# Kernel tuning notes

Measured on AMD Instinct MI355X. Metric: run time of the kernel, lower is better.

The kernel has to match this reference:

```python
import jax, jax.numpy as jnp
import numpy as np

N_NODES = 50000
N_EDGES = 800000
N_GRAPHS = 64
EPS = 1e-12


def setup_inputs() -> dict:
    key = jax.random.key(0)
    ks = jax.random.split(key, 8)
    x = jax.random.normal(ks[0], (N_NODES, 128), dtype=jnp.float32)
    edge_index = jax.random.randint(ks[1], (2, N_EDGES), 0, N_NODES, dtype=jnp.int64)
    batch = jnp.sort(jax.random.randint(ks[2], (N_NODES,), 0, N_GRAPHS, dtype=jnp.int64))
    W1 = jax.random.normal(ks[3], (128, 64), dtype=jnp.float32) * 0.1
    W2 = jax.random.normal(ks[4], (64, 64), dtype=jnp.float32) * 0.1
    W3 = jax.random.normal(ks[5], (64, 64), dtype=jnp.float32) * 0.1
    Wl = jax.random.normal(ks[6], (128, 32), dtype=jnp.float32) * 0.1
    return {
        'x': x, 'edge_index': edge_index, 'batch': batch,
        'W1': W1, 'b1': jnp.zeros((64,), jnp.float32),
        'W2': W2, 'b2': jnp.zeros((64,), jnp.float32),
        'W3': W3, 'b3': jnpp if False else jnp.zeros((64,), jnp.float32),
        'Wl': Wl, 'bl': jnp.zeros((32,), jnp.float32),
    }


def _gcn_conv(h, W, b, src, dst, dinv, enorm, n):
    # PyG GCNConv: D^-1/2 (A+I) D^-1/2 (h W) + b, self-loops included analytically
    hw = h @ W
    agg = jax.ops.segment_sum(hw[src] * enorm[:, None], dst, num_segments=n)
    agg = agg + (dinv * dinv)[:, None] * hw  # self-loop term
    return agg + b


def _norm_relu(h):
    # F.normalize(p=2, dim=1) then relu
    nrm = jnp.sqrt(jnp.sum(h * h, axis=1, keepdims=True))
    return jax.nn.relu(h / jnp.maximum(nrm, EPS))


def reference(x, edge_index, batch, W1, b1, W2, b2, W3, b3, Wl, bl):
    n = x.shape[0]
    src, dst = edge_index[0], edge_index[1]
    # degree with self-loops (counts incoming edges at target, +1 for self-loop)
    deg = jax.ops.segment_sum(jnp.ones((src.shape[0],), x.dtype), dst, num_segments=n) + 1.0
    dinv = 1.0 / jnp.sqrt(deg)
    enorm = dinv[src] * dinv[dst]

    h = _norm_relu(_gcn_conv(x, W1, b1, src, dst, dinv, enorm, n))
    h = _norm_relu(_gcn_conv(h, W2, b2, src, dst, dinv, enorm, n))
    h = _norm_relu(_gcn_conv(h, W3, b3, src, dst, dinv, enorm, n))

    counts = jax.ops.segment_sum(jnp.ones((n,), x.dtype), batch, num_segments=N_GRAPHS)
    x_mean = jax.ops.segment_sum(h, batch, num_segments=N_GRAPHS) / jnp.maximum(counts, 1.0)[:, None]
    x_max = jax.ops.segment_max(h, batch, num_segments=N_GRAPHS)
    x_max = jnp.where(counts[:, None] > 0, x_max, 0.0)  # guard empty graphs

    pooled = jnp.concatenate([x_mean, x_max], axis=-1)  # [B, 2*hidden]
    return pooled @ Wl + bl
```

## Files before the change

kernel.cpp:

```cpp
#include <hip/hip_runtime.h>
#include <hip/hip_bf16.h>

#define N_NODES 50000
#define N_EDGES 800000
#define N_GRAPHS 64
#define HID 64
#define SCAN_NB 196
#define FILL_RANGES 8
#define RANGE_SIZE ((N_NODES + FILL_RANGES - 1) / FILL_RANGES)
#define MM1_BLOCKS ((N_NODES + 63) / 64)
#define FILL_BLOCKS (FILL_RANGES * ((N_EDGES + 255) / 256))

static inline size_t align256(size_t x) { return (x + 255) & ~(size_t)255; }

typedef __attribute__((ext_vector_type(8))) short short8v;
typedef __attribute__((ext_vector_type(4))) float f32x4;

__device__ __forceinline__ unsigned short f2bf(float f) {
    unsigned int u = __float_as_uint(f);
    unsigned int r = (u + 0x7fffu + ((u >> 16) & 1u)) >> 16;
    return (unsigned short)r;
}
__device__ __forceinline__ float bf2f(unsigned short h) {
    return __uint_as_float(((unsigned int)h) << 16);
}

__global__ void zero2(int* __restrict__ a, int na, int* __restrict__ b, int nb) {
    int i = blockIdx.x * blockDim.x + threadIdx.x;
    if (i < na) a[i] = 0;
    else if (i < na + nb) b[i - na] = 0;
}

__global__ void deg_kernel(const int* __restrict__ ei, int* __restrict__ cnt) {
    int e = blockIdx.x * blockDim.x + threadIdx.x;
    if (e < N_EDGES) atomicAdd(&cnt[ei[N_EDGES + e]], 1);
}

__global__ __launch_bounds__(256) void scan_a(const int* __restrict__ cnt,
                                              int* __restrict__ incl,
                                              int* __restrict__ bsum) {
    __shared__ int sd[256];
    int t = threadIdx.x;
    int i = blockIdx.x * 256 + t;
    int v = (i < N_NODES) ? cnt[i] : 0;
    sd[t] = v;
    __syncthreads();
    for (int off = 1; off < 256; off <<= 1) {
        int u = (t >= off) ? sd[t - off] : 0;
        __syncthreads();
        sd[t] += u;
        __syncthreads();
    }
    if (i < N_NODES) incl[i] = sd[t];
    if (t == 255) bsum[blockIdx.x] = sd[255];
}

__global__ __launch_bounds__(384) void scan_b_gstart(const int* __restrict__ bsum,
                                                     int* __restrict__ boff,
                                                     const int* __restrict__ batch,
                                                     int* __restrict__ gstart) {
    __shared__ int sd[256];
    int t = threadIdx.x;
    int v = 0;
    if (t < 256) {
        v = (t < SCAN_NB) ? bsum[t] : 0;
        sd[t] = v;
    }
    __syncthreads();
    for (int off = 1; off < 256; off <<= 1) {
        int u = (t < 256 && t >= off) ? sd[t - off] : 0;
        __syncthreads();
        if (t < 256) sd[t] += u;
        __syncthreads();
    }
    if (t < SCAN_NB) boff[t] = sd[t] - v;
    if (t >= 256 && t - 256 <= N_GRAPHS) {
        int g = t - 256;
        int lo = 0, hi = N_NODES;
        while (lo < hi) {
            int mid = (lo + hi) >> 1;
            if (batch[mid] < g) lo = mid + 1; else hi = mid;
        }
        gstart[g] = lo;
    }
}

__global__ void scan_c(const int* __restrict__ cnt, const int* __restrict__ incl,
                       const int* __restrict__ boff, int* __restrict__ row_ptr,
                       int* __restrict__ fill_ptr, float* __restrict__ dinv) {
    int i = blockIdx.x * blockDim.x + threadIdx.x;
    if (i < N_NODES) {
        int c = cnt[i];
        int run = boff[i >> 8] + incl[i];
        row_ptr[i + 1] = run;
        fill_ptr[i] = run - c;
        dinv[i] = rsqrtf((float)c + 1.0f);
        if (i == 0) row_ptr[0] = 0;
    }
}

__global__ __launch_bounds__(256) void fill_mm1_kernel(const int* __restrict__ ei,
                                                       int* __restrict__ fill_ptr,
                                                       unsigned short* __restrict__ csr_src,
                                                       const float* __restrict__ h,
                                                       const float* __restrict__ W,
                                                       const float* __restrict__ dinv,
                                                       unsigned short* __restrict__ hw2) {
    constexpr int K = 128;
    constexpr int NSTEP = K / 32;
    __shared__ unsigned short sWH[NSTEP * 4 * 64 * 8];
    __shared__ unsigned short sWL[NSTEP * 4 * 64 * 8];
    int tid = threadIdx.x;

    if (blockIdx.x >= MM1_BLOCKS) {
        int fb = blockIdx.x - MM1_BLOCKS;
        int r = fb & (FILL_RANGES - 1);
        int e = (fb >> 3) * 256 + tid;
        if (e >= N_EDGES) return;
        int dst = ei[N_EDGES + e];
        int lo = r * RANGE_SIZE;
        if (dst >= lo && dst < lo + RANGE_SIZE) {
            int src = ei[e];
            int pos = atomicAdd(&fill_ptr[dst], 1);
            csr_src[pos] = (unsigned short)src;
        }
        return;
    }

    int r0 = blockIdx.x * 64;
#pragma unroll 1
    for (int ent = tid; ent < NSTEP * 4 * 64; ent += 256) {
        int lane_e = ent & 63;
        int c = (ent >> 6) & 3;
        int step = ent >> 8;
        int kb = step * 32 + (lane_e >> 4) * 8;
        int n = c * 16 + (lane_e & 15);
#pragma unroll
        for (int j = 0; j < 8; ++j) {
            float f = W[(kb + j) * 64 + n];
            unsigned short hi = f2bf(f);
            sWH[ent * 8 + j] = hi;
            sWL[ent * 8 + j] = f2bf(f - bf2f(hi));
        }
    }
    __syncthreads();

    int lane = tid & 63;
    int wid = tid >> 6;
    int arow = min(r0 + wid * 16 + (lane & 15), N_NODES - 1);
    const float* ap = h + (size_t)arow * K;
    int klane = (lane >> 4) * 8;

    f32x4 acc[4];
#pragma unroll
    for (int c = 0; c < 4; ++c) acc[c] = (f32x4){0.f, 0.f, 0.f, 0.f};

#pragma unroll 1
    for (int step = 0; step < NSTEP; ++step) {
        int kb = step * 32 + klane;
        float4 f0 = *(const float4*)&ap[kb];
        float4 f1 = *(const float4*)&ap[kb + 4];
        float fv[8] = {f0.x, f0.y, f0.z, f0.w, f1.x, f1.y, f1.z, f1.w};
        short8v ahi, alo;
#pragma unroll
        for (int j = 0; j < 8; ++j) {
            unsigned short hi = f2bf(fv[j]);
            ahi[j] = (short)hi;
            alo[j] = (short)f2bf(fv[j] - bf2f(hi));
        }
#pragma unroll
        for (int c = 0; c < 4; ++c) {
            short8v bh = *(const short8v*)&sWH[((step * 4 + c) * 64 + lane) * 8];
            short8v bl = *(const short8v*)&sWL[((step * 4 + c) * 64 + lane) * 8];
            acc[c] = __builtin_amdgcn_mfma_f32_16x16x32_bf16(ahi, bh, acc[c], 0, 0, 0);
            acc[c] = __builtin_amdgcn_mfma_f32_16x16x32_bf16(alo, bh, acc[c], 0, 0, 0);
            acc[c] = __builtin_amdgcn_mfma_f32_16x16x32_bf16(ahi, bl, acc[c], 0, 0, 0);
        }
    }

    int rb = r0 + wid * 16 + (lane >> 4) * 4;
#pragma unroll
    for (int j = 0; j < 4; ++j) {
        int row = rb + j;
        if (row < N_NODES) {
            float dv = dinv[row];
#pragma unroll
            for (int c = 0; c < 4; ++c) {
                hw2[(size_t)row * 64 + c * 16 + (lane & 15)] = f2bf(dv * acc[c][j]);
            }
        }
    }
}

template <int K>
__global__ __launch_bounds__(256) void mfma_matmul(const float* __restrict__ h,
                                                   const float* __restrict__ W,
                                                   const float* __restrict__ dinv,
                                                   unsigned short* __restrict__ hw2) {
    constexpr int NSTEP = K / 32;
    __shared__ unsigned short sWH[NSTEP * 4 * 64 * 8];
    __shared__ unsigned short sWL[NSTEP * 4 * 64 * 8];
    int tid = threadIdx.x;
    int r0 = blockIdx.x * 64;

#pragma unroll 1
    for (int ent = tid; ent < NSTEP * 4 * 64; ent += 256) {
        int lane_e = ent & 63;
        int c = (ent >> 6) & 3;
        int step = ent >> 8;
        int kb = step * 32 + (lane_e >> 4) * 8;
        int n = c * 16 + (lane_e & 15);
#pragma unroll
        for (int j = 0; j < 8; ++j) {
            float f = W[(kb + j) * 64 + n];
            unsigned short hi = f2bf(f);
            sWH[ent * 8 + j] = hi;
            sWL[ent * 8 + j] = f2bf(f - bf2f(hi));
        }
    }
    __syncthreads();

    int lane = tid & 63;
    int wid = tid >> 6;
    int arow = min(r0 + wid * 16 + (lane & 15), N_NODES - 1);
    const float* ap = h + (size_t)arow * K;
    int klane = (lane >> 4) * 8;

    f32x4 acc[4];
#pragma unroll
    for (int c = 0; c < 4; ++c) acc[c] = (f32x4){0.f, 0.f, 0.f, 0.f};

#pragma unroll 1
    for (int step = 0; step < NSTEP; ++step) {
        int kb = step * 32 + klane;
        float4 f0 = *(const float4*)&ap[kb];
        float4 f1 = *(const float4*)&ap[kb + 4];
        float fv[8] = {f0.x, f0.y, f0.z, f0.w, f1.x, f1.y, f1.z, f1.w};
        short8v ahi, alo;
#pragma unroll
        for (int j = 0; j < 8; ++j) {
            unsigned short hi = f2bf(fv[j]);
            ahi[j] = (short)hi;
            alo[j] = (short)f2bf(fv[j] - bf2f(hi));
        }
#pragma unroll
        for (int c = 0; c < 4; ++c) {
            short8v bh = *(const short8v*)&sWH[((step * 4 + c) * 64 + lane) * 8];
            short8v bl = *(const short8v*)&sWL[((step * 4 + c) * 64 + lane) * 8];
            acc[c] = __builtin_amdgcn_mfma_f32_16x16x32_bf16(ahi, bh, acc[c], 0, 0, 0);
            acc[c] = __builtin_amdgcn_mfma_f32_16x16x32_bf16(alo, bh, acc[c], 0, 0, 0);
            acc[c] = __builtin_amdgcn_mfma_f32_16x16x32_bf16(ahi, bl, acc[c], 0, 0, 0);
        }
    }

    int rb = r0 + wid * 16 + (lane >> 4) * 4;
#pragma unroll
    for (int j = 0; j < 4; ++j) {
        int row = rb + j;
        if (row < N_NODES) {
            float dv = dinv[row];
#pragma unroll
            for (int c = 0; c < 4; ++c) {
                hw2[(size_t)row * 64 + c * 16 + (lane & 15)] = f2bf(dv * acc[c][j]);
            }
        }
    }
}

template <bool POOL>
__global__ __launch_bounds__(256) void agg_kernel(const unsigned short* __restrict__ hw2,
                                                  const int* __restrict__ row_ptr,
                                                  const unsigned short* __restrict__ csr_src,
                                                  const float* __restrict__ dinv,
                                                  const float* __restrict__ b,
                                                  float* __restrict__ hout,
                                                  const int* __restrict__ batch,
                                                  float* __restrict__ gsum,
                                                  float* __restrict__ gmax) {
    __shared__ float sh[4][64];
    int tid = threadIdx.x;
    int node = blockIdx.x * 4 + (tid >> 6);
    int lane = tid & 63;
    int grp = lane >> 3;
    int gl  = lane & 7;
    int s = row_ptr[node], e = row_ptr[node + 1];

    float acc[8] = {0.f, 0.f, 0.f, 0.f, 0.f, 0.f, 0.f, 0.f};
    for (int base = s; base < e; base += 64) {
        int nE = min(64, e - base);
        int msrc = (lane < nE) ? (int)csr_src[base + lane] : 0;
#pragma unroll
        for (int rr = 0; rr < 8; ++rr) {
            int i = rr * 8;
            if (i >= nE) break;
            int myi = i + grp;
            int src = __shfl(msrc, myi, 64);
            bool ok = myi < nE;
            int srcx = ok ? src : node;
            short8v v = *(const short8v*)&hw2[(size_t)srcx * 64 + gl * 8];
            if (ok) {
#pragma unroll
                for (int j = 0; j < 8; ++j) acc[j] += bf2f((unsigned short)v[j]);
            }
        }
    }
#pragma unroll
    for (int off = 8; off <= 32; off <<= 1) {
#pragma unroll
        for (int j = 0; j < 8; ++j) acc[j] += __shfl_xor(acc[j], off, 64);
    }
    short8v sv = *(const short8v*)&hw2[(size_t)node * 64 + gl * 8];
#pragma unroll
    for (int j = 0; j < 8; ++j) acc[j] += bf2f((unsigned short)sv[j]);

    float di = dinv[node];
    float4 b0 = *(const float4*)&b[gl * 8];
    float4 b1 = *(const float4*)&b[gl * 8 + 4];
    float val[8];
    val[0] = di * acc[0] + b0.x;
    val[1] = di * acc[1] + b0.y;
    val[2] = di * acc[2] + b0.z;
    val[3] = di * acc[3] + b0.w;
    val[4] = di * acc[4] + b1.x;
    val[5] = di * acc[5] + b1.y;
    val[6] = di * acc[6] + b1.z;
    val[7] = di * acc[7] + b1.w;

    float sq = 0.f;
#pragma unroll
    for (int j = 0; j < 8; ++j) sq += val[j] * val[j];
#pragma unroll
    for (int off = 1; off <= 4; off <<= 1) sq += __shfl_xor(sq, off, 64);
    float inv = 1.0f / fmaxf(sqrtf(sq), 1e-12f);

    if (POOL) {
        if (grp == 0) {
            float4 r0, r1;
            r0.x = fmaxf(val[0] * inv, 0.f);
            r0.y = fmaxf(val[1] * inv, 0.f);
            r0.z = fmaxf(val[2] * inv, 0.f);
            r0.w = fmaxf(val[3] * inv, 0.f);
            r1.x = fmaxf(val[4] * inv, 0.f);
            r1.y = fmaxf(val[5] * inv, 0.f);
            r1.z = fmaxf(val[6] * inv, 0.f);
            r1.w = fmaxf(val[7] * inv, 0.f);
            *(float4*)&sh[tid >> 6][gl * 8] = r0;
            *(float4*)&sh[tid >> 6][gl * 8 + 4] = r1;
        }
        __syncthreads();
        if (tid < 64) {
            int nb = blockIdx.x * 4;
            int gcur = batch[nb];
            float runsum = 0.f, runmax = 0.f;
#pragma unroll
            for (int w = 0; w < 4; ++w) {
                int g = batch[nb + w];
                if (g != gcur) {
                    atomicAdd(&gsum[gcur * 64 + tid], runsum);
                    atomicMax((int*)&gmax[gcur * 64 + tid], __float_as_int(runmax));
                    runsum = 0.f; runmax = 0.f; gcur = g;
                }
                float v = sh[w][tid];
                runsum += v;
                runmax = fmaxf(runmax, v);
            }
            atomicAdd(&gsum[gcur * 64 + tid], runsum);
            atomicMax((int*)&gmax[gcur * 64 + tid], __float_as_int(runmax));
        }
    } else {
        if (grp == 0) {
            float4 r0, r1;
            r0.x = fmaxf(val[0] * inv, 0.f);
            r0.y = fmaxf(val[1] * inv, 0.f);
            r0.z = fmaxf(val[2] * inv, 0.f);
            r0.w = fmaxf(val[3] * inv, 0.f);
            r1.x = fmaxf(val[4] * inv, 0.f);
            r1.y = fmaxf(val[5] * inv, 0.f);
            r1.z = fmaxf(val[6] * inv, 0.f);
            r1.w = fmaxf(val[7] * inv, 0.f);
            *(float4*)&hout[(size_t)node * 64 + gl * 8] = r0;
            *(float4*)&hout[(size_t)node * 64 + gl * 8 + 4] = r1;
        }
    }
}

__global__ __launch_bounds__(128) void linear_kernel(const float* __restrict__ gsum,
                                                     const float* __restrict__ gmax,
                                                     const int* __restrict__ gstart,
                                                     const float* __restrict__ Wl,
                                                     const float* __restrict__ bl,
                                                     float* __restrict__ out) {
    int g = blockIdx.x;
    __shared__ float pooled[128];
    int t = threadIdx.x;
    if (t < 64) {
        int cnt = gstart[g + 1] - gstart[g];
        pooled[t] = gsum[g * 64 + t] / fmaxf((float)cnt, 1.0f);
    } else {
        pooled[t] = gmax[g * 64 + (t - 64)];
    }
    __syncthreads();
    if (t < 32) {
        float acc = bl[t];
#pragma unroll 8
        for (int k = 0; k < 128; ++k) acc += pooled[k] * Wl[k * 32 + t];
        out[g * 32 + t] = acc;
    }
}

extern "C" void kernel_launch(void* const* d_in, const int* in_sizes, int n_in,
                              void* d_out, int out_size, void* d_ws, size_t ws_size,
                              hipStream_t stream) {
    const float* x        = (const float*)d_in[0];
    const int*   ei       = (const int*)d_in[1];
    const int*   batch    = (const int*)d_in[2];
    const float* W1       = (const float*)d_in[3];
    const float* b1       = (const float*)d_in[4];
    const float* W2       = (const float*)d_in[5];
    const float* b2       = (const float*)d_in[6];
    const float* W3       = (const float*)d_in[7];
    const float* b3       = (const float*)d_in[8];
    const float* Wl       = (const float*)d_in[9];
    const float* bl       = (const float*)d_in[10];
    float* out = (float*)d_out;

    char* ws = (char*)d_ws;
    int*   cnt      = (int*)ws;                 ws += align256((size_t)N_NODES * 4);
    int*   incl     = (int*)ws;                 ws += align256((size_t)N_NODES * 4);
    int*   bsum     = (int*)ws;                 ws += align256((size_t)SCAN_NB * 4);
    int*   boff     = (int*)ws;                 ws += align256((size_t)SCAN_NB * 4);
    int*   row_ptr  = (int*)ws;                 ws += align256((size_t)(N_NODES + 1) * 4);
    int*   fill_ptr = (int*)ws;                 ws += align256((size_t)N_NODES * 4);
    float* dinv     = (float*)ws;               ws += align256((size_t)N_NODES * 4);
    int*   gstart   = (int*)ws;                 ws += align256((size_t)(N_GRAPHS + 1) * 4);
    float* gsum     = (float*)ws;               ws += (size_t)N_GRAPHS * 64 * 4;
    float* gmax     = (float*)ws;               ws += align256((size_t)N_GRAPHS * 64 * 4);
    unsigned short* csr_src = (unsigned short*)ws; ws += align256((size_t)N_EDGES * 2);
    unsigned short* hwb = (unsigned short*)ws;  ws += align256((size_t)N_NODES * 64 * 2);
    float* h1       = (float*)ws;               ws += align256((size_t)N_NODES * 64 * 4);
    float* h2       = (float*)ws;               ws += align256((size_t)N_NODES * 64 * 4);

    hipLaunchKernelGGL(zero2, dim3((N_NODES + 2 * N_GRAPHS * 64 + 255) / 256), dim3(256), 0,
                       stream, cnt, N_NODES, (int*)gsum, 2 * N_GRAPHS * 64);
    hipLaunchKernelGGL(deg_kernel, dim3((N_EDGES + 255) / 256), dim3(256), 0, stream, ei, cnt);
    hipLaunchKernelGGL(scan_a, dim3(SCAN_NB), dim3(256), 0, stream, cnt, incl, bsum);
    hipLaunchKernelGGL(scan_b_gstart, dim3(1), dim3(384), 0, stream, bsum, boff, batch, gstart);
    hipLaunchKernelGGL(scan_c, dim3(SCAN_NB), dim3(256), 0, stream,
                       cnt, incl, boff, row_ptr, fill_ptr, dinv);

    const int mm_grid = (N_NODES + 63) / 64;
    const int agg_grid = N_NODES / 4;

    hipLaunchKernelGGL(fill_mm1_kernel, dim3(MM1_BLOCKS + FILL_BLOCKS), dim3(256), 0, stream,
                       ei, fill_ptr, csr_src, x, W1, dinv, hwb);

    hipLaunchKernelGGL((agg_kernel<false>), dim3(agg_grid), dim3(256), 0, stream,
                       hwb, row_ptr, csr_src, dinv, b1, h1, batch, gsum, gmax);
    hipLaunchKernelGGL((mfma_matmul<64>), dim3(mm_grid), dim3(256), 0, stream, h1, W2, dinv, hwb);
    hipLaunchKernelGGL((agg_kernel<false>), dim3(agg_grid), dim3(256), 0, stream,
                       hwb, row_ptr, csr_src, dinv, b2, h2, batch, gsum, gmax);
    hipLaunchKernelGGL((mfma_matmul<64>), dim3(mm_grid), dim3(256), 0, stream, h2, W3, dinv, hwb);
    hipLaunchKernelGGL((agg_kernel<true>), dim3(agg_grid), dim3(256), 0, stream,
                       hwb, row_ptr, csr_src, dinv, b3, (float*)nullptr, batch, gsum, gmax);

    hipLaunchKernelGGL(linear_kernel, dim3(N_GRAPHS), dim3(128), 0, stream,
                       gsum, gmax, gstart, Wl, bl, out);
}
```

Measured before the change: 208.8 us.

## Fuse GCN aggregation with next-layer matmul in one kernel

Merges each layer's aggregation, normalize and ReLU with the following layer's MFMA matmul. Each 1024-thread block aggregates 16 nodes into shared memory, then 4 waves multiply that 16x64 tile by the next weight matrix. This removes the fp32 intermediate h1/h2 round trips through global memory and two kernel launches. In exchange every block re-converts W into shared memory, and the large blocks with a barrier may lower occupancy and make waves wait on the slowest node's neighbor loop.

```diff
diff --git a/kernel.cpp b/kernel.cpp
--- a/kernel.cpp
+++ b/kernel.cpp
@@ -192,19 +192,20 @@
     }
 }
 
-template <int K>
-__global__ __launch_bounds__(256) void mfma_matmul(const float* __restrict__ h,
-                                                   const float* __restrict__ W,
-                                                   const float* __restrict__ dinv,
-                                                   unsigned short* __restrict__ hw2) {
-    constexpr int NSTEP = K / 32;
-    __shared__ unsigned short sWH[NSTEP * 4 * 64 * 8];
-    __shared__ unsigned short sWL[NSTEP * 4 * 64 * 8];
+__global__ __launch_bounds__(1024) void aggmm_kernel(const unsigned short* __restrict__ hw_in,
+                                                     const int* __restrict__ row_ptr,
+                                                     const unsigned short* __restrict__ csr_src,
+                                                     const float* __restrict__ dinv,
+                                                     const float* __restrict__ b,
+                                                     const float* __restrict__ Wn,
+                                                     unsigned short* __restrict__ hw_out) {
+    __shared__ unsigned short sWH[2 * 4 * 64 * 8];
+    __shared__ unsigned short sWL[2 * 4 * 64 * 8];
+    __shared__ float hlds[16 * 68];
     int tid = threadIdx.x;
-    int r0 = blockIdx.x * 64;
-
-#pragma unroll 1
-    for (int ent = tid; ent < NSTEP * 4 * 64; ent += 256) {
+
+    if (tid < 512) {
+        int ent = tid;
         int lane_e = ent & 63;
         int c = (ent >> 6) & 3;
         int step = ent >> 8;
@@ -212,74 +213,15 @@
         int n = c * 16 + (lane_e & 15);
 #pragma unroll
         for (int j = 0; j < 8; ++j) {
-            float f = W[(kb + j) * 64 + n];
+            float f = Wn[(kb + j) * 64 + n];
             unsigned short hi = f2bf(f);
             sWH[ent * 8 + j] = hi;
             sWL[ent * 8 + j] = f2bf(f - bf2f(hi));
         }
     }
-    __syncthreads();
-
-    int lane = tid & 63;
+
     int wid = tid >> 6;
-    int arow = min(r0 + wid * 16 + (lane & 15), N_NODES - 1);
-    const float* ap = h + (size_t)arow * K;
-    int klane = (lane >> 4) * 8;
-
-    f32x4 acc[4];
-#pragma unroll
-    for (int c = 0; c < 4; ++c) acc[c] = (f32x4){0.f, 0.f, 0.f, 0.f};
-
-#pragma unroll 1
-    for (int step = 0; step < NSTEP; ++step) {
-        int kb = step * 32 + klane;
-        float4 f0 = *(const float4*)&ap[kb];
-        float4 f1 = *(const float4*)&ap[kb + 4];
-        float fv[8] = {f0.x, f0.y, f0.z, f0.w, f1.x, f1.y, f1.z, f1.w};
-        short8v ahi, alo;
-#pragma unroll
-        for (int j = 0; j < 8; ++j) {
-            unsigned short hi = f2bf(fv[j]);
-            ahi[j] = (short)hi;
-            alo[j] = (short)f2bf(fv[j] - bf2f(hi));
-        }
-#pragma unroll
-        for (int c = 0; c < 4; ++c) {
-            short8v bh = *(const short8v*)&sWH[((step * 4 + c) * 64 + lane) * 8];
-            short8v bl = *(const short8v*)&sWL[((step * 4 + c) * 64 + lane) * 8];
-            acc[c] = __builtin_amdgcn_mfma_f32_16x16x32_bf16(ahi, bh, acc[c], 0, 0, 0);
-            acc[c] = __builtin_amdgcn_mfma_f32_16x16x32_bf16(alo, bh, acc[c], 0, 0, 0);
-            acc[c] = __builtin_amdgcn_mfma_f32_16x16x32_bf16(ahi, bl, acc[c], 0, 0, 0);
-        }
-    }
-
-    int rb = r0 + wid * 16 + (lane >> 4) * 4;
-#pragma unroll
-    for (int j = 0; j < 4; ++j) {
-        int row = rb + j;
-        if (row < N_NODES) {
-            float dv = dinv[row];
-#pragma unroll
-            for (int c = 0; c < 4; ++c) {
-                hw2[(size_t)row * 64 + c * 16 + (lane & 15)] = f2bf(dv * acc[c][j]);
-            }
-        }
-    }
-}
-
-template <bool POOL>
-__global__ __launch_bounds__(256) void agg_kernel(const unsigned short* __restrict__ hw2,
-                                                  const int* __restrict__ row_ptr,
-                                                  const unsigned short* __restrict__ csr_src,
-                                                  const float* __restrict__ dinv,
-                                                  const float* __restrict__ b,
-                                                  float* __restrict__ hout,
-                                                  const int* __restrict__ batch,
-                                                  float* __restrict__ gsum,
-                                                  float* __restrict__ gmax) {
-    __shared__ float sh[4][64];
-    int tid = threadIdx.x;
-    int node = blockIdx.x * 4 + (tid >> 6);
+    int node = blockIdx.x * 16 + wid;
     int lane = tid & 63;
     int grp = lane >> 3;
     int gl  = lane & 7;
@@ -297,7 +239,7 @@
             int src = __shfl(msrc, myi, 64);
             bool ok = myi < nE;
             int srcx = ok ? src : node;
-            short8v v = *(const short8v*)&hw2[(size_t)srcx * 64 + gl * 8];
+            short8v v = *(const short8v*)&hw_in[(size_t)srcx * 64 + gl * 8];
             if (ok) {
 #pragma unroll
                 for (int j = 0; j < 8; ++j) acc[j] += bf2f((unsigned short)v[j]);
@@ -309,7 +251,7 @@
 #pragma unroll
         for (int j = 0; j < 8; ++j) acc[j] += __shfl_xor(acc[j], off, 64);
     }
-    short8v sv = *(const short8v*)&hw2[(size_t)node * 64 + gl * 8];
+    short8v sv = *(const short8v*)&hw_in[(size_t)node * 64 + gl * 8];
 #pragma unroll
     for (int j = 0; j < 8; ++j) acc[j] += bf2f((unsigned short)sv[j]);
 
@@ -333,54 +275,146 @@
     for (int off = 1; off <= 4; off <<= 1) sq += __shfl_xor(sq, off, 64);
     float inv = 1.0f / fmaxf(sqrtf(sq), 1e-12f);
 
-    if (POOL) {
-        if (grp == 0) {
-            float4 r0, r1;
-            r0.x = fmaxf(val[0] * inv, 0.f);
-            r0.y = fmaxf(val[1] * inv, 0.f);
-            r0.z = fmaxf(val[2] * inv, 0.f);
-            r0.w = fmaxf(val[3] * inv, 0.f);
-            r1.x = fmaxf(val[4] * inv, 0.f);
-            r1.y = fmaxf(val[5] * inv, 0.f);
-            r1.z = fmaxf(val[6] * inv, 0.f);
-            r1.w = fmaxf(val[7] * inv, 0.f);
-            *(float4*)&sh[tid >> 6][gl * 8] = r0;
-            *(float4*)&sh[tid >> 6][gl * 8 + 4] = r1;
-        }
-        __syncthreads();
-        if (tid < 64) {
-            int nb = blockIdx.x * 4;
-            int gcur = batch[nb];
-            float runsum = 0.f, runmax = 0.f;
-#pragma unroll
-            for (int w = 0; w < 4; ++w) {
-                int g = batch[nb + w];
-                if (g != gcur) {
-                    atomicAdd(&gsum[gcur * 64 + tid], runsum);
-                    atomicMax((int*)&gmax[gcur * 64 + tid], __float_as_int(runmax));
-                    runsum = 0.f; runmax = 0.f; gcur = g;
-                }
-                float v = sh[w][tid];
-                runsum += v;
-                runmax = fmaxf(runmax, v);
+    if (grp == 0) {
+        float4 r0, r1;
+        r0.x = fmaxf(val[0] * inv, 0.f);
+        r0.y = fmaxf(val[1] * inv, 0.f);
+        r0.z = fmaxf(val[2] * inv, 0.f);
+        r0.w = fmaxf(val[3] * inv, 0.f);
+        r1.x = fmaxf(val[4] * inv, 0.f);
+        r1.y = fmaxf(val[5] * inv, 0.f);
+        r1.z = fmaxf(val[6] * inv, 0.f);
+        r1.w = fmaxf(val[7] * inv, 0.f);
+        *(float4*)&hlds[wid * 68 + gl * 8] = r0;
+        *(float4*)&hlds[wid * 68 + gl * 8 + 4] = r1;
+    }
+    __syncthreads();
+
+    if (wid < 4) {
+        int klane = (lane >> 4) * 8;
+        f32x4 macc = (f32x4){0.f, 0.f, 0.f, 0.f};
+#pragma unroll
+        for (int step = 0; step < 2; ++step) {
+            const float* hr = &hlds[(lane & 15) * 68 + step * 32 + klane];
+            short8v ahi, alo;
+#pragma unroll
+            for (int j = 0; j < 8; ++j) {
+                float f = hr[j];
+                unsigned short hi = f2bf(f);
+                ahi[j] = (short)hi;
+                alo[j] = (short)f2bf(f - bf2f(hi));
             }
-            atomicAdd(&gsum[gcur * 64 + tid], runsum);
-            atomicMax((int*)&gmax[gcur * 64 + tid], __float_as_int(runmax));
-        }
-    } else {
-        if (grp == 0) {
-            float4 r0, r1;
-            r0.x = fmaxf(val[0] * inv, 0.f);
-            r0.y = fmaxf(val[1] * inv, 0.f);
-            r0.z = fmaxf(val[2] * inv, 0.f);
-            r0.w = fmaxf(val[3] * inv, 0.f);
-            r1.x = fmaxf(val[4] * inv, 0.f);
-            r1.y = fmaxf(val[5] * inv, 0.f);
-            r1.z = fmaxf(val[6] * inv, 0.f);
-            r1.w = fmaxf(val[7] * inv, 0.f);
-            *(float4*)&hout[(size_t)node * 64 + gl * 8] = r0;
-            *(float4*)&hout[(size_t)node * 64 + gl * 8 + 4] = r1;
-        }
+            short8v bh = *(const short8v*)&sWH[((step * 4 + wid) * 64 + lane) * 8];
+            short8v bl = *(const short8v*)&sWL[((step * 4 + wid) * 64 + lane) * 8];
+            macc = __builtin_amdgcn_mfma_f32_16x16x32_bf16(ahi, bh, macc, 0, 0, 0);
+            macc = __builtin_amdgcn_mfma_f32_16x16x32_bf16(alo, bh, macc, 0, 0, 0);
+            macc = __builtin_amdgcn_mfma_f32_16x16x32_bf16(ahi, bl, macc, 0, 0, 0);
+        }
+        int rb = blockIdx.x * 16 + (lane >> 4) * 4;
+#pragma unroll
+        for (int j = 0; j < 4; ++j) {
+            int row = rb + j;
+            hw_out[(size_t)row * 64 + wid * 16 + (lane & 15)] = f2bf(dinv[row] * macc[j]);
+        }
+    }
+}
+
+__global__ __launch_bounds__(256) void agg_pool_kernel(const unsigned short* __restrict__ hw2,
+                                                       const int* __restrict__ row_ptr,
+                                                       const unsigned short* __restrict__ csr_src,
+                                                       const float* __restrict__ dinv,
+                                                       const float* __restrict__ b,
+                                                       const int* __restrict__ batch,
+                                                       float* __restrict__ gsum,
+                                                       float* __restrict__ gmax) {
+    __shared__ float sh[4][64];
+    int tid = threadIdx.x;
+    int node = blockIdx.x * 4 + (tid >> 6);
+    int lane = tid & 63;
+    int grp = lane >> 3;
+    int gl  = lane & 7;
+    int s = row_ptr[node], e = row_ptr[node + 1];
+
+    float acc[8] = {0.f, 0.f, 0.f, 0.f, 0.f, 0.f, 0.f, 0.f};
+    for (int base = s; base < e; base += 64) {
+        int nE = min(64, e - base);
+        int msrc = (lane < nE) ? (int)csr_src[base + lane] : 0;
+#pragma unroll
+        for (int rr = 0; rr < 8; ++rr) {
+            int i = rr * 8;
+            if (i >= nE) break;
+            int myi = i + grp;
+            int src = __shfl(msrc, myi, 64);
+            bool ok = myi < nE;
+            int srcx = ok ? src : node;
+            short8v v = *(const short8v*)&hw2[(size_t)srcx * 64 + gl * 8];
+            if (ok) {
+#pragma unroll
+                for (int j = 0; j < 8; ++j) acc[j] += bf2f((unsigned short)v[j]);
+            }
+        }
+    }
+#pragma unroll
+    for (int off = 8; off <= 32; off <<= 1) {
+#pragma unroll
+        for (int j = 0; j < 8; ++j) acc[j] += __shfl_xor(acc[j], off, 64);
+    }
+    short8v sv = *(const short8v*)&hw2[(size_t)node * 64 + gl * 8];
+#pragma unroll
+    for (int j = 0; j < 8; ++j) acc[j] += bf2f((unsigned short)sv[j]);
+
+    float di = dinv[node];
+    float4 b0 = *(const float4*)&b[gl * 8];
+    float4 b1 = *(const float4*)&b[gl * 8 + 4];
+    float val[8];
+    val[0] = di * acc[0] + b0.x;
+    val[1] = di * acc[1] + b0.y;
+    val[2] = di * acc[2] + b0.z;
+    val[3] = di * acc[3] + b0.w;
+    val[4] = di * acc[4] + b1.x;
+    val[5] = di * acc[5] + b1.y;
+    val[6] = di * acc[6] + b1.z;
+    val[7] = di * acc[7] + b1.w;
+
+    float sq = 0.f;
+#pragma unroll
+    for (int j = 0; j < 8; ++j) sq += val[j] * val[j];
+#pragma unroll
+    for (int off = 1; off <= 4; off <<= 1) sq += __shfl_xor(sq, off, 64);
+    float inv = 1.0f / fmaxf(sqrtf(sq), 1e-12f);
+
+    if (grp == 0) {
+        float4 r0, r1;
+        r0.x = fmaxf(val[0] * inv, 0.f);
+        r0.y = fmaxf(val[1] * inv, 0.f);
+        r0.z = fmaxf(val[2] * inv, 0.f);
+        r0.w = fmaxf(val[3] * inv, 0.f);
+        r1.x = fmaxf(val[4] * inv, 0.f);
+        r1.y = fmaxf(val[5] * inv, 0.f);
+        r1.z = fmaxf(val[6] * inv, 0.f);
+        r1.w = fmaxf(val[7] * inv, 0.f);
+        *(float4*)&sh[tid >> 6][gl * 8] = r0;
+        *(float4*)&sh[tid >> 6][gl * 8 + 4] = r1;
+    }
+    __syncthreads();
+    if (tid < 64) {
+        int nb = blockIdx.x * 4;
+        int gcur = batch[nb];
+        float runsum = 0.f, runmax = 0.f;
+#pragma unroll
+        for (int w = 0; w < 4; ++w) {
+            int g = batch[nb + w];
+            if (g != gcur) {
+                atomicAdd(&gsum[gcur * 64 + tid], runsum);
+                atomicMax((int*)&gmax[gcur * 64 + tid], __float_as_int(runmax));
+                runsum = 0.f; runmax = 0.f; gcur = g;
+            }
+            float v = sh[w][tid];
+            runsum += v;
+            runmax = fmaxf(runmax, v);
+        }
+        atomicAdd(&gsum[gcur * 64 + tid], runsum);
+        atomicMax((int*)&gmax[gcur * 64 + tid], __float_as_int(runmax));
     }
 }
 
@@ -436,9 +470,8 @@
     float* gsum     = (float*)ws;               ws += (size_t)N_GRAPHS * 64 * 4;
     float* gmax     = (float*)ws;               ws += align256((size_t)N_GRAPHS * 64 * 4);
     unsigned short* csr_src = (unsigned short*)ws; ws += align256((size_t)N_EDGES * 2);
+    unsigned short* hwa = (unsigned short*)ws;  ws += align256((size_t)N_NODES * 64 * 2);
     unsigned short* hwb = (unsigned short*)ws;  ws += align256((size_t)N_NODES * 64 * 2);
-    float* h1       = (float*)ws;               ws += align256((size_t)N_NODES * 64 * 4);
-    float* h2       = (float*)ws;               ws += align256((size_t)N_NODES * 64 * 4);
 
     hipLaunchKernelGGL(zero2, dim3((N_NODES + 2 * N_GRAPHS * 64 + 255) / 256), dim3(256), 0,
                        stream, cnt, N_NODES, (int*)gsum, 2 * N_GRAPHS * 64);
@@ -448,20 +481,18 @@
     hipLaunchKernelGGL(scan_c, dim3(SCAN_NB), dim3(256), 0, stream,
                        cnt, incl, boff, row_ptr, fill_ptr, dinv);
 
-    const int mm_grid = (N_NODES + 63) / 64;
-    const int agg_grid = N_NODES / 4;
-
     hipLaunchKernelGGL(fill_mm1_kernel, dim3(MM1_BLOCKS + FILL_BLOCKS), dim3(256), 0, stream,
-                       ei, fill_ptr, csr_src, x, W1, dinv, hwb);
-
-    hipLaunchKernelGGL((agg_kernel<false>), dim3(agg_grid), dim3(256), 0, stream,
-                       hwb, row_ptr, csr_src, dinv, b1, h1, batch, gsum, gmax);
-    hipLaunchKernelGGL((mfma_matmul<64>), dim3(mm_grid), dim3(256), 0, stream, h1, W2, dinv, hwb);
-    hipLaunchKernelGGL((agg_kernel<false>), dim3(agg_grid), dim3(256), 0, stream,
-                       hwb, row_ptr, csr_src, dinv, b2, h2, batch, gsum, gmax);
-    hipLaunchKernelGGL((mfma_matmul<64>), dim3(mm_grid), dim3(256), 0, stream, h2, W3, dinv, hwb);
-    hipLaunchKernelGGL((agg_kernel<true>), dim3(agg_grid), dim3(256), 0, stream,
-                       hwb, row_ptr, csr_src, dinv, b3, (float*)nullptr, batch, gsum, gmax);
+                       ei, fill_ptr, csr_src, x, W1, dinv, hwa);
+
+    const int aggmm_grid = N_NODES / 16;
+    const int aggp_grid  = N_NODES / 4;
+
+    hipLaunchKernelGGL(aggmm_kernel, dim3(aggmm_grid), dim3(1024), 0, stream,
+                       hwa, row_ptr, csr_src, dinv, b1, W2, hwb);
+    hipLaunchKernelGGL(aggmm_kernel, dim3(aggmm_grid), dim3(1024), 0, stream,
+                       hwb, row_ptr, csr_src, dinv, b2, W3, hwa);
+    hipLaunchKernelGGL(agg_pool_kernel, dim3(aggp_grid), dim3(256), 0, stream,
+                       hwa, row_ptr, csr_src, dinv, b3, batch, gsum, gmax);
 
     hipLaunchKernelGGL(linear_kernel, dim3(N_GRAPHS), dim3(128), 0, stream,
                        gsum, gmax, gstart, Wl, bl, out);
```

After: 206.9 us. No clear change (-0.9%).
